# Optimization experiments

Measured on AMD Instinct MI355X. Metric: run time of the kernel, lower is better.

The kernel has to match this reference:

```python
import jax, jax.numpy as jnp
import numpy as np

T, N, FI, FO = 32, 2048, 64, 64  # timesteps, nodes, in_feats, out_feats (= TopK k)


def _uniform(key, shape, stdv):
    return jax.random.uniform(key, shape, minval=-stdv, maxval=stdv, dtype=jnp.float32)


def setup_inputs() -> dict:
    key = jax.random.key(0)
    ks = jax.random.split(key, 12)
    A_list = jax.random.uniform(ks[0], (T, N, N), dtype=jnp.float32)  # stands in for A_hat per step
    Nodes_list = jax.random.normal(ks[1], (T, N, FI), dtype=jnp.float32)
    nodes_mask_list = jnp.zeros((T, N), dtype=jnp.float32)  # additive mask (0 = unmasked)
    s_w = 1.0 / np.sqrt(FO)   # reset_param uses 1/sqrt(size(1))
    s_g = 1.0 / np.sqrt(FI)   # gate W/U are [FI,FI]
    s_s = 1.0 / np.sqrt(FI)   # scorer reset uses 1/sqrt(size(0))
    GCN_init_weights = _uniform(ks[2], (FI, FO), s_w)
    scorer = _uniform(ks[3], (FI, 1), s_s)
    Wu = _uniform(ks[4], (FI, FI), s_g); Uu = _uniform(ks[5], (FI, FI), s_g)
    Wr = _uniform(ks[6], (FI, FI), s_g); Ur = _uniform(ks[7], (FI, FI), s_g)
    Wh = _uniform(ks[8], (FI, FI), s_g); Uh = _uniform(ks[9], (FI, FI), s_g)
    bu = jnp.zeros((FI, FO), jnp.float32)
    br = jnp.zeros((FI, FO), jnp.float32)
    bh = jnp.zeros((FI, FO), jnp.float32)
    return {"A_list": A_list, "Nodes_list": Nodes_list, "nodes_mask_list": nodes_mask_list,
            "GCN_init_weights": GCN_init_weights, "scorer": scorer,
            "Wu": Wu, "Uu": Uu, "bu": bu, "Wr": Wr, "Ur": Ur, "br": br,
            "Wh": Wh, "Uh": Uh, "bh": bh}


def reference(A_list, Nodes_list, nodes_mask_list, GCN_init_weights, scorer,
              Wu, Uu, bu, Wr, Ur, br, Wh, Uh, bh):
    k = GCN_init_weights.shape[1]  # TopK k == out_feats (static)

    def topk_embed(X, mask):
        # scores = X @ scorer / ||scorer|| + mask ; select top-k nodes
        scores = (X @ scorer).ravel() / jnp.linalg.norm(scorer) + mask  # [N]
        vals, idx = jax.lax.top_k(scores, k)                            # [k]
        sel = X[idx]                                                    # [k, FI]
        return (sel * jnp.tanh(vals)[:, None]).T                        # [FI, k]

    def step(Q, inp):
        Ahat, X, mask = inp
        z = topk_embed(X, mask)                          # [FI, FO]
        u = jax.nn.sigmoid(Wu @ z + Uu @ Q + bu)         # update gate
        r = jax.nn.sigmoid(Wr @ z + Ur @ Q + br)         # reset gate
        h = jax.nn.relu(Wh @ z + Uh @ (r * Q) + bh)      # candidate
        Qn = (1.0 - u) * Q + u * h                       # evolved GCN weights
        out = jax.nn.relu(Ahat @ (X @ Qn))               # [N, FO]
        return Qn, out

    _, out_seq = jax.lax.scan(step, GCN_init_weights,
                              (A_list, Nodes_list, nodes_mask_list))
    return out_seq  # [T, N, FO]
```

## Files before the change

### kernel.cpp

```cpp
#include <hip/hip_runtime.h>
#include <hip/hip_bf16.h>
#include <math.h>

#define TT 32
#define NN 2048
#define FF 64

typedef float f32x4 __attribute__((ext_vector_type(4)));
typedef __bf16 bf16x8 __attribute__((ext_vector_type(8)));
typedef unsigned short u16x8 __attribute__((ext_vector_type(8)));

__device__ __forceinline__ unsigned short f2bf(float f) {
    __bf16 h = (__bf16)f;
    return __builtin_bit_cast(unsigned short, h);
}

__global__ __launch_bounds__(256) void score_kernel(
    const float* __restrict__ X, const float* __restrict__ mask,
    const float* __restrict__ scorer,
    double* __restrict__ scores, unsigned short* __restrict__ Xbf)
{
    const int t = blockIdx.y, tid = threadIdx.x;
    const int n = blockIdx.x * 256 + tid;
    __shared__ float scf[64];
    if (tid < 64) scf[tid] = scorer[tid];
    __syncthreads();

    double nrm = 0.0;
#pragma unroll
    for (int f = 0; f < 64; ++f) nrm += (double)scf[f] * (double)scf[f];
    const double inv = 1.0 / sqrt(nrm);

    const float* xr = X + ((size_t)t * NN + n) * FF;
    unsigned short* xo = Xbf + ((size_t)t * NN + n) * FF;
    double s = 0.0;
#pragma unroll
    for (int f = 0; f < 64; f += 4) {
        float4 v = *(const float4*)(xr + f);
        s += (double)v.x * (double)scf[f]   + (double)v.y * (double)scf[f+1]
           + (double)v.z * (double)scf[f+2] + (double)v.w * (double)scf[f+3];
        ushort4 pk = make_ushort4(f2bf(v.x), f2bf(v.y), f2bf(v.z), f2bf(v.w));
        *(ushort4*)(xo + f) = pk;
    }
    scores[t * NN + n] = s * inv + (double)mask[t * NN + n];
}

__global__ __launch_bounds__(1024) void select_kernel(
    const double* __restrict__ scores,
    int* __restrict__ tkidx, float* __restrict__ tkval)
{
    const int t = blockIdx.x, tid = threadIdx.x;
    const int lane = tid & 63, w = tid >> 6;
    __shared__ double sk[1024];
    __shared__ int    si[1024];

    double v0 = scores[t * NN + (w << 7) + lane];
    double v1 = scores[t * NN + (w << 7) + 64 + lane];
    int    i0 = (w << 7) + lane;
    int    i1 = (w << 7) + 64 + lane;

#define BETTER(av, ai, bv, bi) ((av) > (bv) || ((av) == (bv) && (ai) < (bi)))
#pragma unroll
    for (int k = 2; k <= 128; k <<= 1) {
#pragma unroll
        for (int j = 64; j > 0; j >>= 1) {
            if (j > (k >> 1)) continue;
            if (j == 64) {
                const bool ib = BETTER(v0, i0, v1, i1);
                if (!ib) {
                    const double tv = v0; v0 = v1; v1 = tv;
                    const int ti = i0; i0 = i1; i1 = ti;
                }
            } else {
                {
                    const double pv = __shfl_xor(v0, j);
                    const int    pi = __shfl_xor(i0, j);
                    const bool lower = (lane & j) == 0;
                    const bool up = ((lane & k) == 0);
                    const bool ib = BETTER(v0, i0, pv, pi);
                    const bool keep = (up == lower) ? ib : !ib;
                    if (!keep) { v0 = pv; i0 = pi; }
                }
                {
                    const double pv = __shfl_xor(v1, j);
                    const int    pi = __shfl_xor(i1, j);
                    const bool lower = (lane & j) == 0;
                    const bool up = (k == 64) ? false : ((lane & k) == 0);
                    const bool ib = BETTER(v1, i1, pv, pi);
                    const bool keep = (up == lower) ? ib : !ib;
                    if (!keep) { v1 = pv; i1 = pi; }
                }
            }
        }
    }
#undef BETTER
    sk[(w << 6) + lane] = v0;
    si[(w << 6) + lane] = i0;
    __syncthreads();

    for (int k = 2; k <= 1024; k <<= 1) {
        for (int jj = k >> 1; jj > 0; jj >>= 1) {
            const int i = tid, l = i ^ jj;
            if (l > i) {
                const double a = sk[i], b2 = sk[l];
                const int ai = si[i], bi2 = si[l];
                const bool ib = (a > b2) || (a == b2 && ai < bi2);
                const bool keep = ((i & k) == 0) ? ib : !ib;
                if (!keep) {
                    sk[i] = b2; sk[l] = a;
                    si[i] = bi2; si[l] = ai;
                }
            }
            __syncthreads();
        }
    }

    if (tid < 64) {
        tkidx[t * 64 + tid] = si[tid];
        tkval[t * 64 + tid] = tanhf((float)sk[tid]);
    }
}

__global__ __launch_bounds__(256) void qchain_kernel(
    const float* __restrict__ Q0,
    const float* __restrict__ Uu, const float* __restrict__ Ur,
    const float* __restrict__ Uh,
    const float* __restrict__ Wu, const float* __restrict__ Wr,
    const float* __restrict__ Wh,
    const float* __restrict__ bu, const float* __restrict__ br,
    const float* __restrict__ bh,
    const int* __restrict__ tkidx, const float* __restrict__ tkval,
    const float* __restrict__ X, unsigned short* __restrict__ Qtr)
{
    const int j = blockIdx.x, tid = threadIdx.x;
    const int w = tid >> 6, l = tid & 63;
    const int i = (w << 4) + (l & 15);
    const int fq = l >> 4, fb = fq << 4;

    __shared__ __align__(16) float zsh[TT][64];
    __shared__ __align__(16) float wzl[3 * TT * 64];
    __shared__ __align__(16) float qd[2][64];
    __shared__ __align__(16) float rr[64];

    {
        const int tt = tid >> 3, p8 = (tid & 7) << 3;
        const int idxt = tkidx[tt * 64 + j];
        const float th = tkval[tt * 64 + j];
        const float* xr = X + ((size_t)tt * NN + idxt) * FF + p8;
        float4 v0 = *(const float4*)(xr);
        float4 v1 = *(const float4*)(xr + 4);
        zsh[tt][p8]     = v0.x * th; zsh[tt][p8 + 1] = v0.y * th;
        zsh[tt][p8 + 2] = v0.z * th; zsh[tt][p8 + 3] = v0.w * th;
        zsh[tt][p8 + 4] = v1.x * th; zsh[tt][p8 + 5] = v1.y * th;
        zsh[tt][p8 + 6] = v1.z * th; zsh[tt][p8 + 7] = v1.w * th;
    }

    float uu[16], ur[16], uh[16], wu[16], wr[16], wh[16];
#pragma unroll
    for (int e = 0; e < 16; e += 4) {
        float4 a = *(const float4*)(Uu + i * 64 + fb + e);
        uu[e] = a.x; uu[e+1] = a.y; uu[e+2] = a.z; uu[e+3] = a.w;
        float4 c = *(const float4*)(Ur + i * 64 + fb + e);
        ur[e] = c.x; ur[e+1] = c.y; ur[e+2] = c.z; ur[e+3] = c.w;
        float4 d = *(const float4*)(Uh + i * 64 + fb + e);
        uh[e] = d.x; uh[e+1] = d.y; uh[e+2] = d.z; uh[e+3] = d.w;
        float4 p = *(const float4*)(Wu + i * 64 + fb + e);
        wu[e] = p.x; wu[e+1] = p.y; wu[e+2] = p.z; wu[e+3] = p.w;
        float4 s = *(const float4*)(Wr + i * 64 + fb + e);
        wr[e] = s.x; wr[e+1] = s.y; wr[e+2] = s.z; wr[e+3] = s.w;
        float4 g = *(const float4*)(Wh + i * 64 + fb + e);
        wh[e] = g.x; wh[e+1] = g.y; wh[e+2] = g.z; wh[e+3] = g.w;
    }
    const float bui = bu[i * 64 + j];
    const float bri = br[i * 64 + j];
    const float bhi = bh[i * 64 + j];
    if (tid < 64) qd[0][tid] = Q0[tid * 64 + j];
    __syncthreads();

    for (int t = 0; t < TT; ++t) {
        float z16[16];
#pragma unroll
        for (int e = 0; e < 16; e += 4) {
            f32x4 z = *(const f32x4*)(&zsh[t][fb + e]);
            z16[e] = z[0]; z16[e+1] = z[1]; z16[e+2] = z[2]; z16[e+3] = z[3];
        }
        float pu = 0.f, pr = 0.f, ph = 0.f;
#pragma unroll
        for (int e = 0; e < 16; ++e) {
            pu += wu[e] * z16[e];
            pr += wr[e] * z16[e];
            ph += wh[e] * z16[e];
        }
        pu += __shfl_xor(pu, 16); pu += __shfl_xor(pu, 32);
        pr += __shfl_xor(pr, 16); pr += __shfl_xor(pr, 32);
        ph += __shfl_xor(ph, 16); ph += __shfl_xor(ph, 32);
        if (fq == 0) {
            wzl[(0 * TT + t) * 64 + i] = pu;
            wzl[(1 * TT + t) * 64 + i] = pr;
            wzl[(2 * TT + t) * 64 + i] = ph;
        }
    }
    __syncthreads();

    int cur = 0;
    for (int t = 0; t < TT; ++t) {
        float q16[16];
#pragma unroll
        for (int e = 0; e < 16; e += 4) {
            f32x4 v = *(const f32x4*)(&qd[cur][fb + e]);
            q16[e] = v[0]; q16[e+1] = v[1]; q16[e+2] = v[2]; q16[e+3] = v[3];
        }
        float su = 0.f, sr = 0.f;
#pragma unroll
        for (int e = 0; e < 16; ++e) { su += uu[e] * q16[e]; sr += ur[e] * q16[e]; }
        su += __shfl_xor(su, 16); su += __shfl_xor(su, 32);
        sr += __shfl_xor(sr, 16); sr += __shfl_xor(sr, 32);
        const float u_ = 1.f / (1.f + expf(-(su + wzl[(0 * TT + t) * 64 + i] + bui)));
        const float r_ = 1.f / (1.f + expf(-(sr + wzl[(1 * TT + t) * 64 + i] + bri)));
        if (fq == 0) rr[i] = r_;
        __syncthreads();
        float sh = 0.f;
#pragma unroll
        for (int e = 0; e < 16; e += 4) {
            f32x4 v = *(const f32x4*)(&rr[fb + e]);
            sh += uh[e]   * (v[0] * q16[e]);
            sh += uh[e+1] * (v[1] * q16[e+1]);
            sh += uh[e+2] * (v[2] * q16[e+2]);
            sh += uh[e+3] * (v[3] * q16[e+3]);
        }
        sh += __shfl_xor(sh, 16); sh += __shfl_xor(sh, 32);
        float hv = sh + wzl[(2 * TT + t) * 64 + i] + bhi;
        hv = hv > 0.f ? hv : 0.f;
        const float qi = qd[cur][i];
        const float qn = (1.f - u_) * qi + u_ * hv;
        if (fq == 0) {
            qd[cur ^ 1][i] = qn;
            Qtr[(size_t)t * 4096 + j * 64 + i] = f2bf(qn);
        }
        __syncthreads();
        cur ^= 1;
    }
}

__global__ __launch_bounds__(256) void ymfma_kernel(
    const unsigned short* __restrict__ Xbf, const unsigned short* __restrict__ Qtr,
    unsigned short* __restrict__ Ytr)
{
    __shared__ __align__(16) unsigned char Qb[8192];
    const int t = blockIdx.y, tid = threadIdx.x;
    const int n0 = blockIdx.x * 256;
    const int lane = tid & 63, w = tid >> 6;
    const int lr = lane & 15, lq = lane >> 4;

    const unsigned short* Qp = Qtr + (size_t)t * 4096;
#pragma unroll
    for (int q2 = 0; q2 < 2; ++q2) {
        const int j = (w << 4) + (q2 << 3) + (lane >> 3);
        const unsigned short* g = Qp + (size_t)j * 64 + (((lane & 7) ^ (j & 7)) << 3);
        __builtin_amdgcn_global_load_lds(
            (const __attribute__((address_space(1))) void*)g,
            (__attribute__((address_space(3))) void*)
                (&Qb[((w << 4) + (q2 << 3)) << 7]), 16, 0, 0);
    }
    __syncthreads();

    f32x4 acc[4][4];
#pragma unroll
    for (int jt = 0; jt < 4; ++jt)
#pragma unroll
        for (int nt = 0; nt < 4; ++nt) acc[jt][nt] = (f32x4){0.f, 0.f, 0.f, 0.f};

#pragma unroll
    for (int ks = 0; ks < 2; ++ks) {
        bf16x8 af[4], bf[4];
#pragma unroll
        for (int jt = 0; jt < 4; ++jt) {
            const int j = (jt << 4) + lr;
            const int x = ((ks << 2) + lq) ^ (j & 7);
            af[jt] = *(const bf16x8*)(&Qb[(j << 7) + (x << 4)]);
        }
#pragma unroll
        for (int nt = 0; nt < 4; ++nt) {
            const int n = n0 + (w << 6) + (nt << 4) + lr;
            bf[nt] = __builtin_bit_cast(bf16x8,
                *(const uint4*)(Xbf + ((size_t)t * NN + n) * FF + (ks << 5) + (lq << 3)));
        }
#pragma unroll
        for (int jt = 0; jt < 4; ++jt)
#pragma unroll
            for (int nt = 0; nt < 4; ++nt)
                acc[jt][nt] = __builtin_amdgcn_mfma_f32_16x16x32_bf16(
                    af[jt], bf[nt], acc[jt][nt], 0, 0, 0);
    }

#pragma unroll
    for (int jt = 0; jt < 4; ++jt)
#pragma unroll
        for (int nt = 0; nt < 4; ++nt) {
            const int nn = n0 + (w << 6) + (nt << 4) + lr;
#pragma unroll
            for (int rg = 0; rg < 4; ++rg) {
                const int j = (jt << 4) + (lq << 2) + rg;
                Ytr[(size_t)t * FF * NN + (size_t)j * NN + nn] = f2bf(acc[jt][nt][rg]);
            }
        }
}

__global__ __launch_bounds__(256, 4) void gemm_kernel(
    const float* __restrict__ A, const unsigned short* __restrict__ Ytr,
    float* __restrict__ out)
{
    __shared__ __align__(16) unsigned char Abuf[16384];
    __shared__ __align__(16) unsigned char Bbuf[8192];
    const int tid = threadIdx.x;
    const int bid = blockIdx.x;
    const int xcd = bid & 7, li = bid >> 3;
    const int t = (xcd << 2) + (li >> 5);
    const int m0 = (li & 31) * 64;
    const int lane = tid & 63, w = tid >> 6;
    const int lr = lane & 15, lq = lane >> 4;

    const float* Ap = A + (size_t)t * NN * NN + (size_t)m0 * NN;
    const unsigned short* Yp = Ytr + (size_t)t * FF * NN;

    f32x4 acc[4];
#pragma unroll
    for (int nt = 0; nt < 4; ++nt) acc[nt] = (f32x4){0.f, 0.f, 0.f, 0.f};

    for (int kt = 0; kt < 32; ++kt) {
        const int kk = kt << 6;
#pragma unroll
        for (int q = 0; q < 4; ++q) {
            const int row = (w << 4) + (q << 2) + lq;
            const float* g = Ap + (size_t)row * NN + kk + ((lr ^ (row & 7)) << 2);
            __builtin_amdgcn_global_load_lds(
                (const __attribute__((address_space(1))) void*)g,
                (__attribute__((address_space(3))) void*)
                    (&Abuf[((w << 4) + (q << 2)) << 8]), 16, 0, 0);
        }
#pragma unroll
        for (int q = 0; q < 2; ++q) {
            const int j = (w << 4) + (q << 3) + (lane >> 3);
            const unsigned short* g = Yp + (size_t)j * NN + kk
                                    + (((lane & 7) ^ (j & 7)) << 3);
            __builtin_amdgcn_global_load_lds(
                (const __attribute__((address_space(1))) void*)g,
                (__attribute__((address_space(3))) void*)
                    (&Bbuf[((w << 4) + (q << 3)) << 7]), 16, 0, 0);
        }
        __syncthreads();
#pragma unroll
        for (int ks = 0; ks < 2; ++ks) {
            const int r = (w << 4) + lr;
            const int c0 = ((ks << 3) + (lq << 1)) ^ (lr & 7);
            const int c1 = ((ks << 3) + (lq << 1) + 1) ^ (lr & 7);
            const f32x4 a0 = *(const f32x4*)(&Abuf[(r << 8) + (c0 << 4)]);
            const f32x4 a1 = *(const f32x4*)(&Abuf[(r << 8) + (c1 << 4)]);
            bf16x8 af;
            af[0] = (__bf16)a0[0]; af[1] = (__bf16)a0[1];
            af[2] = (__bf16)a0[2]; af[3] = (__bf16)a0[3];
            af[4] = (__bf16)a1[0]; af[5] = (__bf16)a1[1];
            af[6] = (__bf16)a1[2]; af[7] = (__bf16)a1[3];
#pragma unroll
            for (int nt = 0; nt < 4; ++nt) {
                const int j = (nt << 4) + lr;
                const int x = ((ks << 2) + lq) ^ (j & 7);
                const bf16x8 bf = *(const bf16x8*)(&Bbuf[(j << 7) + (x << 4)]);
                acc[nt] = __builtin_amdgcn_mfma_f32_16x16x32_bf16(
                    af, bf, acc[nt], 0, 0, 0);
            }
        }
        __syncthreads();
    }

#pragma unroll
    for (int nt = 0; nt < 4; ++nt) {
        const int row0 = m0 + (w << 4) + (lq << 2);
        const int col = (nt << 4) + lr;
#pragma unroll
        for (int rg = 0; rg < 4; ++rg) {
            const float v = acc[nt][rg];
            out[((size_t)t * NN + (row0 + rg)) * FF + col] = v > 0.f ? v : 0.f;
        }
    }
}

extern "C" void kernel_launch(void* const* d_in, const int* in_sizes, int n_in,
                              void* d_out, int out_size, void* d_ws, size_t ws_size,
                              hipStream_t stream) {
    const float* A      = (const float*)d_in[0];
    const float* X      = (const float*)d_in[1];
    const float* mask   = (const float*)d_in[2];
    const float* Q0     = (const float*)d_in[3];
    const float* scorer = (const float*)d_in[4];
    const float* Wu     = (const float*)d_in[5];
    const float* Uu     = (const float*)d_in[6];
    const float* bu     = (const float*)d_in[7];
    const float* Wr     = (const float*)d_in[8];
    const float* Ur     = (const float*)d_in[9];
    const float* br     = (const float*)d_in[10];
    const float* Wh     = (const float*)d_in[11];
    const float* Uh     = (const float*)d_in[12];
    const float* bh     = (const float*)d_in[13];
    float* out = (float*)d_out;

    float* ws = (float*)d_ws;
    double* scores        = (double*)ws;
    int*    tkidx         = (int*)(ws + 131072);
    float*  tkval         = ws + 133120;
    unsigned short* Qtr   = (unsigned short*)(ws + 135168);
    unsigned short* Xbf   = (unsigned short*)(ws + 200704);
    unsigned short* Ytr   = (unsigned short*)(ws + 2297856);

    score_kernel<<<dim3(8, TT), 256, 0, stream>>>(X, mask, scorer, scores, Xbf);
    select_kernel<<<TT, 1024, 0, stream>>>(scores, tkidx, tkval);
    qchain_kernel<<<FF, 256, 0, stream>>>(Q0, Uu, Ur, Uh, Wu, Wr, Wh,
                                          bu, br, bh, tkidx, tkval, X, Qtr);
    ymfma_kernel<<<dim3(8, TT), 256, 0, stream>>>(Xbf, Qtr, Ytr);
    gemm_kernel<<<1024, 256, 0, stream>>>(A, Ytr, out);
}
```

Baseline: 203.6 us.

## Replace full shared-memory bitonic sort with wave-level top-64 merge tree

The full 1024-element bitonic sort in shared memory, with a block barrier after every compare-exchange stage, is replaced by a tree merge of the per-wave sorted 64-element lists. Each round pairs two sorted lists, keeps the better half with a reversed-order compare, then runs a 6-step shuffle bitonic merge inside the wave. Only four rounds with two barriers each are needed instead of dozens of barriers. This relies on each wave's list already being sorted descending, and on only the top 64 being needed.

```diff
diff --git a/kernel.cpp b/kernel.cpp
--- a/kernel.cpp
+++ b/kernel.cpp
@@ -93,27 +93,41 @@
             }
         }
     }
-#undef BETTER
     sk[(w << 6) + lane] = v0;
     si[(w << 6) + lane] = i0;
     __syncthreads();
 
-    for (int k = 2; k <= 1024; k <<= 1) {
-        for (int jj = k >> 1; jj > 0; jj >>= 1) {
-            const int i = tid, l = i ^ jj;
-            if (l > i) {
-                const double a = sk[i], b2 = sk[l];
-                const int ai = si[i], bi2 = si[l];
-                const bool ib = (a > b2) || (a == b2 && ai < bi2);
-                const bool keep = ((i & k) == 0) ? ib : !ib;
-                if (!keep) {
-                    sk[i] = b2; sk[l] = a;
-                    si[i] = bi2; si[l] = ai;
-                }
+#pragma unroll
+    for (int round = 0; round < 4; ++round) {
+        const int nl = 8 >> round;
+        double cv = 0.0; int ci = 0;
+        const bool active = (w < nl);
+        if (active) {
+            const int la = (w << 1), lb = (w << 1) + 1;
+            const double av = sk[(la << 6) + lane];
+            const int    ai = si[(la << 6) + lane];
+            const double bv = sk[(lb << 6) + 63 - lane];
+            const int    bi = si[(lb << 6) + 63 - lane];
+            if (BETTER(av, ai, bv, bi)) { cv = av; ci = ai; }
+            else                        { cv = bv; ci = bi; }
+#pragma unroll
+            for (int j = 32; j > 0; j >>= 1) {
+                const double pv = __shfl_xor(cv, j);
+                const int    pi = __shfl_xor(ci, j);
+                const bool lower = (lane & j) == 0;
+                const bool ib = BETTER(cv, ci, pv, pi);
+                const bool keep = lower ? ib : !ib;
+                if (!keep) { cv = pv; ci = pi; }
             }
-            __syncthreads();
-        }
-    }
+        }
+        __syncthreads();
+        if (active) {
+            sk[(w << 6) + lane] = cv;
+            si[(w << 6) + lane] = ci;
+        }
+        __syncthreads();
+    }
+#undef BETTER
 
     if (tid < 64) {
         tkidx[t * 64 + tid] = si[tid];
```

New measurement: 191.1 us, median of 2. -6.2%, faster.
